# Kernel optimization log

Measured on AMD Instinct MI355X. Metric: run time of the kernel, lower is better.

## Reference

```python
import jax, jax.numpy as jnp
import numpy as np

B, S, H, V, T, NS, NB, NSW = 16, 200, 400, 25000, 8, 30, 3, 36


def setup_inputs() -> dict:
    key = jax.random.key(0)
    ks = jax.random.split(key, 12)
    return {
        "encoded_hidden": jax.random.normal(ks[0], (1, B, H), jnp.float32),
        "encoded_outputs": jax.random.normal(ks[1], (B, S, H), jnp.float32),
        "story": jax.random.randint(ks[2], (B, S), 0, V),
        "target_batches": jax.random.randint(ks[3], (B, NS, T), 0, V),
        "slot_dom_idx": jax.random.randint(ks[4], (NS,), 0, NSW),
        "slot_slot_idx": jax.random.randint(ks[5], (NS,), 0, NSW),
        "emb_W": jax.random.normal(ks[6], (V, H), jnp.float32) * 0.05,
        "slot_emb_W": jax.random.normal(ks[7], (NSW, H), jnp.float32) * 0.1,
        "gru_W_ih": jax.random.normal(ks[8], (3 * H, H), jnp.float32) * 0.05,
        "gru_W_hh": jax.random.normal(ks[9], (3 * H, H), jnp.float32) * 0.05,
        "gru_b_ih": jnp.zeros((3 * H,), jnp.float32),
        "gru_b_hh": jnp.zeros((3 * H,), jnp.float32),
        "W_ratio_w": jax.random.normal(ks[10], (1, 3 * H), jnp.float32) * 0.05,
        "W_ratio_b": jnp.zeros((1,), jnp.float32),
        "W_gate_w": jax.random.normal(ks[11], (NB, H), jnp.float32) * 0.05,
        "W_gate_b": jnp.zeros((NB,), jnp.float32),
    }


def reference(encoded_hidden, encoded_outputs, story, target_batches,
              slot_dom_idx, slot_slot_idx, emb_W, slot_emb_W,
              gru_W_ih, gru_W_hh, gru_b_ih, gru_b_hh,
              W_ratio_w, W_ratio_b, W_gate_w, W_gate_b):
    b, s, h = encoded_outputs.shape
    ns = slot_dom_idx.shape[0]
    v = emb_W.shape[0]
    t = target_batches.shape[2]
    bs = ns * b  # flattened slot*batch dim (parallel decode over slots)

    # slot embedding = domain_emb + slot_emb, broadcast over batch
    slot_emb = slot_emb_W[slot_dom_idx] + slot_emb_W[slot_slot_idx]        # [ns,h]
    dec_in0 = jnp.broadcast_to(slot_emb[:, None, :], (ns, b, h)).reshape(bs, h)
    h0 = jnp.tile(encoded_hidden[0], (ns, 1))                              # [bs,h]
    enc = jnp.tile(encoded_outputs, (ns, 1, 1))                            # [bs,s,h]
    pad_mask = jnp.tile(story == 0, (ns, 1))                               # [bs,s]
    story_rep = jnp.tile(story, (ns, 1))                                   # [bs,s]
    # teacher forcing targets, slot-major flatten: [bs, t]
    tf = jnp.transpose(target_batches, (1, 0, 2)).reshape(bs, t)
    rows = jnp.arange(bs)

    def gru_cell(x, hid):
        gx = x @ gru_W_ih.T + gru_b_ih
        gh = hid @ gru_W_hh.T + gru_b_hh
        r = jax.nn.sigmoid(gx[:, :h] + gh[:, :h])
        z = jax.nn.sigmoid(gx[:, h:2 * h] + gh[:, h:2 * h])
        n = jnp.tanh(gx[:, 2 * h:] + r * gh[:, 2 * h:])
        return (1.0 - z) * n + z * hid

    def step(carry, tgt_t):
        hid, x = carry
        hid = gru_cell(x, hid)                                             # [bs,h]
        scores = jnp.einsum('bh,bsh->bs', hid, enc)
        scores = jnp.where(pad_mask, -jnp.inf, scores)
        prob = jax.nn.softmax(scores, axis=1)                              # [bs,s]
        ctx = jnp.einsum('bs,bsh->bh', prob, enc)                          # [bs,h]
        p_vocab = jax.nn.softmax(hid @ emb_W.T, axis=1)                    # [bs,v]
        switch = jax.nn.sigmoid(
            jnp.concatenate([hid, ctx, x], axis=-1) @ W_ratio_w.T + W_ratio_b)  # [bs,1]
        p_ctx = jnp.zeros((bs, v), p_vocab.dtype).at[rows[:, None], story_rep].add(prob)
        final = (1.0 - switch) * p_ctx + switch * p_vocab                  # [bs,v]
        x_next = emb_W[tgt_t]                                              # teacher forcing
        return (hid, x_next), (final, ctx)

    (_, _), (finals, ctxs) = jax.lax.scan(step, (h0, dec_in0), tf.T)
    all_point = jnp.transpose(finals.reshape(t, ns, b, v), (1, 2, 0, 3))   # [ns,b,t,v]
    all_gate = (ctxs[0] @ W_gate_w.T + W_gate_b).reshape(ns, b, -1)        # [ns,b,nb_gate]
    return all_point, all_gate
```

## Files before the change

kernel.cpp:

```cpp
#include <hip/hip_runtime.h>
#include <math.h>

#define B_   16
#define S_   200
#define H_   400
#define V_   25000
#define T_   8
#define NS_  30
#define NB_  3
#define BS_  480

#define KP_  448
#define MP_  512
#define NP_  25088
#define NG_  1280
#define MA_  3840
#define NVT_ (NP_/128)
#define PSL_ 200

typedef unsigned short u16;
typedef __attribute__((ext_vector_type(4))) float f32x4;
typedef __attribute__((ext_vector_type(8))) short short8;

__device__ __forceinline__ u16 f2bf(float f) {
    unsigned u = __float_as_uint(f);
    u += 0x7FFFu + ((u >> 16) & 1u);
    return (u16)(u >> 16);
}
__device__ __forceinline__ float bf2f(u16 v) {
    return __uint_as_float(((unsigned)v) << 16);
}
__device__ __forceinline__ float sigm(float x) {
    return 1.f / (1.f + __expf(-x));
}
__device__ __forceinline__ float ftanh(float x) {
    float e2 = __expf(2.f * x);
    return 1.f - 2.f / (e2 + 1.f);
}
__device__ __forceinline__ float wred_sum(float v) {
    v += __shfl_xor(v, 32); v += __shfl_xor(v, 16); v += __shfl_xor(v, 8);
    v += __shfl_xor(v, 4);  v += __shfl_xor(v, 2);  v += __shfl_xor(v, 1);
    return v;
}
__device__ __forceinline__ float wred_max(float v) {
    v = fmaxf(v, __shfl_xor(v, 32)); v = fmaxf(v, __shfl_xor(v, 16));
    v = fmaxf(v, __shfl_xor(v, 8));  v = fmaxf(v, __shfl_xor(v, 4));
    v = fmaxf(v, __shfl_xor(v, 2));  v = fmaxf(v, __shfl_xor(v, 1));
    return v;
}
__device__ __forceinline__ void gload_lds16(const void* g, void* l) {
    __builtin_amdgcn_global_load_lds(
        (const __attribute__((address_space(1))) void*)g,
        (__attribute__((address_space(3))) void*)l, 16, 0, 0);
}

__device__ __forceinline__ void tile128(const u16* __restrict__ A, const u16* __restrict__ Bw,
                                        float* __restrict__ C, int m0, int n0, int Mlim, int Nlim,
                                        u16* As, u16* Bs, int tid) {
    const int wid = tid >> 6, lane = tid & 63;
    const int wr = wid >> 1, wc = wid & 1;
    f32x4 acc[4][4] = {};
    const int lcol = ((lane & 7) ^ ((lane >> 3) & 7)) * 8;
    const int lr = lane & 15, lg = lane >> 4, lx = lane & 7;
    const int sA0 = (lg ^ lx) * 8, sA1 = ((4 + lg) ^ lx) * 8;
    const u16* Ag = A + (size_t)(m0 + wid * 32 + (lane >> 3)) * KP_ + lcol;
    const u16* Bg = Bw + (size_t)(n0 + wid * 32 + (lane >> 3)) * KP_ + lcol;

    for (int kt = 0; kt < 7; ++kt) {
        const int k0 = kt * 64;
        #pragma unroll
        for (int is = 0; is < 4; ++is) {
            gload_lds16(Ag + (size_t)is * 8 * KP_ + k0, &As[(wid * 32 + is * 8) * 64]);
            gload_lds16(Bg + (size_t)is * 8 * KP_ + k0, &Bs[(wid * 32 + is * 8) * 64]);
        }
        __syncthreads();
        short8 af[4][2], bfr[4][2];
        #pragma unroll
        for (int i = 0; i < 4; ++i) {
            int ra = (wr * 64 + i * 16 + lr) * 64;
            af[i][0] = *reinterpret_cast<const short8*>(&As[ra + sA0]);
            af[i][1] = *reinterpret_cast<const short8*>(&As[ra + sA1]);
            int rb = (wc * 64 + i * 16 + lr) * 64;
            bfr[i][0] = *reinterpret_cast<const short8*>(&Bs[rb + sA0]);
            bfr[i][1] = *reinterpret_cast<const short8*>(&Bs[rb + sA1]);
        }
        #pragma unroll
        for (int h = 0; h < 2; ++h)
            #pragma unroll
            for (int i = 0; i < 4; ++i)
                #pragma unroll
                for (int j = 0; j < 4; ++j)
                    acc[i][j] = __builtin_amdgcn_mfma_f32_16x16x32_bf16(
                        af[i][h], bfr[j][h], acc[i][j], 0, 0, 0);
        __syncthreads();
    }
    const int m_base = m0 + wr * 64 + lg * 4;
    const int n_base = n0 + wc * 64 + lr;
    #pragma unroll
    for (int i = 0; i < 4; ++i)
        #pragma unroll
        for (int r = 0; r < 4; ++r) {
            int m = m_base + i * 16 + r;
            if (m >= Mlim) continue;
            #pragma unroll
            for (int j = 0; j < 4; ++j) {
                int n = n_base + j * 16;
                if (n < Nlim) C[(size_t)m * Nlim + n] = acc[i][j][r];
            }
        }
}

__global__ void prep_all(const float* __restrict__ eh, const float* __restrict__ embW,
                         const float* __restrict__ Wih, const float* __restrict__ Whh,
                         const float* __restrict__ sembW, const int* __restrict__ tb,
                         const int* __restrict__ dom, const int* __restrict__ sli,
                         float* __restrict__ hid, u16* __restrict__ Ab,
                         u16* __restrict__ Bb, u16* __restrict__ Wihb, u16* __restrict__ Whhb,
                         float* __restrict__ x_all, u16* __restrict__ Xb_all) {
    const int R0 = MP_ * KP_;
    const int CB = NP_ * (KP_ / 8), CG = NG_ * (KP_ / 8);
    const int R1 = R0 + CB + 2 * CG;
    const int R2 = R1 + MA_ * (KP_ / 8);
    int i = blockIdx.x * 256 + threadIdx.x;
    if (i < R0) {
        int row = i / KP_, d = i - row * KP_;
        u16 v = 0;
        if (row < BS_ && d < H_) {
            float h = eh[(row % B_) * H_ + d];
            hid[row * H_ + d] = h;
            v = f2bf(h);
        }
        Ab[i] = v;
    } else if (i < R1) {
        int j = i - R0;
        const float* src; u16* dst; int rows;
        if (j < CB) { src = embW; dst = Bb; rows = V_; }
        else if (j < CB + CG) { src = Wih; dst = Wihb; rows = 3 * H_; j -= CB; }
        else { src = Whh; dst = Whhb; rows = 3 * H_; j -= CB + CG; }
        int row = j / (KP_ / 8), c8 = (j - row * (KP_ / 8)) * 8;
        short8 o = {};
        if (row < rows && c8 < H_) {
            const float4* s = reinterpret_cast<const float4*>(src + (size_t)row * H_ + c8);
            float4 a = s[0], b = s[1];
            o[0] = (short)f2bf(a.x); o[1] = (short)f2bf(a.y);
            o[2] = (short)f2bf(a.z); o[3] = (short)f2bf(a.w);
            o[4] = (short)f2bf(b.x); o[5] = (short)f2bf(b.y);
            o[6] = (short)f2bf(b.z); o[7] = (short)f2bf(b.w);
        }
        *reinterpret_cast<short8*>(dst + (size_t)row * KP_ + c8) = o;
    } else if (i < R2) {
        int j = i - R1;
        int row = j / (KP_ / 8), c8 = (j - row * (KP_ / 8)) * 8;
        int t = row / BS_, r = row - t * BS_;
        int batch = r % B_, slot = r / B_;
        short8 o = {};
        if (c8 < H_) {
            float4 a, b;
            if (t == 0) {
                const float4* s0 = reinterpret_cast<const float4*>(sembW + dom[slot] * H_ + c8);
                const float4* s1 = reinterpret_cast<const float4*>(sembW + sli[slot] * H_ + c8);
                float4 x0 = s0[0], x1 = s0[1], y0 = s1[0], y1 = s1[1];
                a = make_float4(x0.x + y0.x, x0.y + y0.y, x0.z + y0.z, x0.w + y0.w);
                b = make_float4(x1.x + y1.x, x1.y + y1.y, x1.z + y1.z, x1.w + y1.w);
            } else {
                int tok = tb[(batch * NS_ + slot) * T_ + (t - 1)];
                const float4* s = reinterpret_cast<const float4*>(embW + (size_t)tok * H_ + c8);
                a = s[0]; b = s[1];
            }
            o[0] = (short)f2bf(a.x); o[1] = (short)f2bf(a.y);
            o[2] = (short)f2bf(a.z); o[3] = (short)f2bf(a.w);
            o[4] = (short)f2bf(b.x); o[5] = (short)f2bf(b.y);
            o[6] = (short)f2bf(b.z); o[7] = (short)f2bf(b.w);
            *reinterpret_cast<float4*>(x_all + (size_t)row * H_ + c8) = a;
            *reinterpret_cast<float4*>(x_all + (size_t)row * H_ + c8 + 4) = b;
        }
        *reinterpret_cast<short8*>(Xb_all + (size_t)row * KP_ + c8) = o;
    }
}

__global__ __launch_bounds__(256)
void gemm_setup(const u16* __restrict__ Xb_all, const u16* __restrict__ Abuf,
                const u16* __restrict__ Wihb, const u16* __restrict__ Whhb,
                float* __restrict__ gx_all, float* __restrict__ gh) {
    __shared__ u16 As[128 * 64];
    __shared__ u16 Bs[128 * 64];
    const int tid = threadIdx.x;
    const bool mainp = blockIdx.y < 4;
    const int m0 = (mainp ? blockIdx.y : blockIdx.y - 4) * 128;
    const int n0 = blockIdx.x * 128;
    if (mainp)
        tile128(Xb_all, Wihb, gx_all, m0, n0, MA_, 3 * H_, As, Bs, tid);
    else
        tile128(Abuf, Whhb, gh, m0, n0, BS_, 3 * H_, As, Bs, tid);
}

__global__ __launch_bounds__(256, 2)
void vocab_gh(const u16* __restrict__ A, const u16* __restrict__ Bb,
              const u16* __restrict__ Whhb, u16* __restrict__ pb,
              float* __restrict__ psum, float* __restrict__ gh,
              const u16* __restrict__ Xb_all, const u16* __restrict__ Wihb,
              float* __restrict__ gx_all) {
    __shared__ u16 As[256 * 64];
    __shared__ u16 Bs[2][128 * 64];
    __shared__ float sred[2][256];
    const int bid = blockIdx.x;
    const int tid = threadIdx.x;

    if (bid >= 412) {
        const int e = bid - 412;
        const int mt = 4 + e / 10, nt = e % 10;
        tile128(Xb_all, Wihb, gx_all, mt * 128, nt * 128, MA_, 3 * H_,
                As, (u16*)&Bs[0][0], tid);
        return;
    }

    const int xcd = bid & 7, idx = bid >> 3;
    const int lin = (xcd < 4) ? (xcd * 52 + idx) : (208 + (xcd - 4) * 51 + idx);
    const int ntall = lin >> 1, mt = lin & 1;
    const bool isv = (ntall < NVT_);
    const int n0 = (isv ? ntall : ntall - NVT_) * 128;
    const int m0 = mt * 256;
    const u16* Bsrc = isv ? Bb : Whhb;

    const int wid = tid >> 6, lane = tid & 63;
    const int wr = wid >> 1, wc = wid & 1;
    f32x4 acc[8][4] = {};
    const int lcol = ((lane & 7) ^ ((lane >> 3) & 7)) * 8;
    const int lr = lane & 15, lg = lane >> 4, lx = lane & 7;
    const int sA0 = (lg ^ lx) * 8, sA1 = ((4 + lg) ^ lx) * 8;
    const u16* Ag = A + (size_t)(m0 + wid * 64 + (lane >> 3)) * KP_ + lcol;
    const u16* Bg = Bsrc + (size_t)(n0 + wid * 32 + (lane >> 3)) * KP_ + lcol;

    #pragma unroll
    for (int is = 0; is < 4; ++is)
        gload_lds16(Bg + (size_t)is * 8 * KP_, &Bs[0][(wid * 32 + is * 8) * 64]);

    for (int kt = 0; kt < 7; ++kt) {
        const int k0 = kt * 64, cur = kt & 1;
        #pragma unroll
        for (int is = 0; is < 8; ++is)
            gload_lds16(Ag + (size_t)is * 8 * KP_ + k0, &As[(wid * 64 + is * 8) * 64]);
        if (kt < 6) {
            #pragma unroll
            for (int is = 0; is < 4; ++is)
                gload_lds16(Bg + (size_t)is * 8 * KP_ + k0 + 64,
                            &Bs[cur ^ 1][(wid * 32 + is * 8) * 64]);
            asm volatile("s_waitcnt vmcnt(4)" ::: "memory");
        } else {
            asm volatile("s_waitcnt vmcnt(0)" ::: "memory");
        }
        __builtin_amdgcn_sched_barrier(0);
        __builtin_amdgcn_s_barrier();
        const u16* Bsl = Bs[cur];
        #pragma unroll
        for (int h = 0; h < 2; ++h) {
            const int sA = h ? sA1 : sA0;
            short8 af[8], bf[4];
            #pragma unroll
            for (int i = 0; i < 8; ++i)
                af[i] = *reinterpret_cast<const short8*>(&As[(wr * 128 + i * 16 + lr) * 64 + sA]);
            #pragma unroll
            for (int j = 0; j < 4; ++j)
                bf[j] = *reinterpret_cast<const short8*>(&Bsl[(wc * 64 + j * 16 + lr) * 64 + sA]);
            #pragma unroll
            for (int i = 0; i < 8; ++i)
                #pragma unroll
                for (int j = 0; j < 4; ++j)
                    acc[i][j] = __builtin_amdgcn_mfma_f32_16x16x32_bf16(
                        af[i], bf[j], acc[i][j], 0, 0, 0);
        }
        __builtin_amdgcn_s_barrier();
    }

    const int m_base = m0 + wr * 128 + lg * 4;
    const int n_base = n0 + wc * 64 + lr;
    if (isv) {
        #pragma unroll
        for (int i = 0; i < 8; ++i) {
            #pragma unroll
            for (int r = 0; r < 4; ++r) {
                int m = m_base + i * 16 + r;
                float js = 0.f;
                #pragma unroll
                for (int j = 0; j < 4; ++j) {
                    int n = n_base + j * 16;
                    float e = __expf(acc[i][j][r]);
                    if (m < BS_ && n < V_) {
                        pb[(size_t)m * V_ + n] = f2bf(e);
                        js += e;
                    }
                }
                js += __shfl_xor(js, 1);
                js += __shfl_xor(js, 2);
                js += __shfl_xor(js, 4);
                js += __shfl_xor(js, 8);
                if ((lane & 15) == 0) sred[wc][m - m0] = js;
            }
        }
        __syncthreads();
        {
            int m = m0 + tid;
            psum[(size_t)m * PSL_ + ntall] = sred[0][tid] + sred[1][tid];
        }
    } else {
        #pragma unroll
        for (int i = 0; i < 8; ++i)
            #pragma unroll
            for (int r = 0; r < 4; ++r) {
                int m = m_base + i * 16 + r;
                if (m >= BS_) continue;
                #pragma unroll
                for (int j = 0; j < 4; ++j) {
                    int n = n_base + j * 16;
                    if (n < 3 * H_) gh[(size_t)m * 3 * H_ + n] = acc[i][j][r];
                }
            }
    }
}

__global__ __launch_bounds__(256)
void attn_fin(const float* __restrict__ gx_all, const float* __restrict__ gh,
              const float* __restrict__ bih, const float* __restrict__ bhh,
              float* __restrict__ hid, u16* __restrict__ Ab,
              const float* __restrict__ x_all,
              const float* __restrict__ enc, const int* __restrict__ story,
              const float* __restrict__ Wr, const float* __restrict__ Wrb,
              const float* __restrict__ Wg, const float* __restrict__ Wgb,
              float* __restrict__ prob_cur, float* __restrict__ sw_cur,
              float* __restrict__ gate_out,
              float* __restrict__ out, const u16* __restrict__ pb,
              const float* __restrict__ psum, const float* __restrict__ sw_prev,
              const float* __restrict__ prob_prev, int t) {
    const int bid = blockIdx.x;
    const int lin = (bid & 7) * 120 + (bid >> 3);
    const int work = lin >> 1, kind = lin & 1;
    const int tid = threadIdx.x, w = tid >> 6, l = tid & 63;
    __shared__ __align__(16) float hs[H_];
    __shared__ __align__(16) float xs[H_];
    __shared__ __align__(16) float cs[H_];
    __shared__ __align__(16) float cpart[4][H_];
    __shared__ float sc[S_];
    __shared__ float red[16];

    if (kind == 1) {
        if (t == 0) return;
        const int row = work, batch = row % B_;
        float rs = (tid < NVT_) ? psum[(size_t)row * PSL_ + tid] : 0.f;
        rs = wred_sum(rs);
        if (l == 0) red[w] = rs;
        __syncthreads();
        float denom = red[0] + red[1] + red[2] + red[3];
        float swv = sw_prev[row];
        float scl = swv / denom;
        const u16* ps = pb + (size_t)row * V_;
        float* p = out + ((size_t)row * T_ + (t - 1)) * V_;
        for (int v = tid * 8; v < V_; v += 256 * 8) {
            short8 in = *reinterpret_cast<const short8*>(ps + v);
            float4 o0, o1;
            o0.x = bf2f((u16)in[0]) * scl; o0.y = bf2f((u16)in[1]) * scl;
            o0.z = bf2f((u16)in[2]) * scl; o0.w = bf2f((u16)in[3]) * scl;
            o1.x = bf2f((u16)in[4]) * scl; o1.y = bf2f((u16)in[5]) * scl;
            o1.z = bf2f((u16)in[6]) * scl; o1.w = bf2f((u16)in[7]) * scl;
            *reinterpret_cast<float4*>(p + v) = o0;
            *reinterpret_cast<float4*>(p + v + 4) = o1;
        }
        __syncthreads();
        float om = 1.f - swv;
        for (int s = tid; s < S_; s += 256) {
            int tok = story[batch * S_ + s];
            atomicAdd(p + tok, om * prob_prev[(size_t)row * S_ + s]);
        }
        return;
    }

    const int batch = work / 30, slot = work - batch * 30;
    const int row = slot * B_ + batch;

    const float* gxr = gx_all + ((size_t)t * BS_ + row) * 3 * H_;
    const float* ghr = gh + (size_t)row * 3 * H_;
    const float* xr  = x_all + ((size_t)t * BS_ + row) * H_;
    for (int d = tid; d < H_; d += 256) {
        float r = sigm(gxr[d] + bih[d] + ghr[d] + bhh[d]);
        float z = sigm(gxr[H_ + d] + bih[H_ + d] + ghr[H_ + d] + bhh[H_ + d]);
        float n = ftanh(gxr[2 * H_ + d] + bih[2 * H_ + d] + r * (ghr[2 * H_ + d] + bhh[2 * H_ + d]));
        float h = (1.f - z) * n + z * hid[(size_t)row * H_ + d];
        hs[d] = h;
        hid[(size_t)row * H_ + d] = h;
        Ab[(size_t)row * KP_ + d] = f2bf(h);
        xs[d] = xr[d];
    }
    __syncthreads();

    const float* encb = enc + (size_t)batch * S_ * H_;
    {
        float4 hv1 = *reinterpret_cast<const float4*>(&hs[l * 4]);
        float4 hv2 = make_float4(0.f, 0.f, 0.f, 0.f);
        if (l < 36) hv2 = *reinterpret_cast<const float4*>(&hs[256 + l * 4]);
        for (int k = 0; k < 50; k += 2) {
            int s0 = w * 50 + k;
            const float4* e0 = reinterpret_cast<const float4*>(encb + (size_t)s0 * H_);
            const float4* e1 = reinterpret_cast<const float4*>(encb + (size_t)(s0 + 1) * H_);
            float4 ev0 = e0[l], ev1 = e1[l];
            float p0 = ev0.x * hv1.x + ev0.y * hv1.y + ev0.z * hv1.z + ev0.w * hv1.w;
            float p1 = ev1.x * hv1.x + ev1.y * hv1.y + ev1.z * hv1.z + ev1.w * hv1.w;
            if (l < 36) {
                float4 f0 = e0[64 + l], f1 = e1[64 + l];
                p0 += f0.x * hv2.x + f0.y * hv2.y + f0.z * hv2.z + f0.w * hv2.w;
                p1 += f1.x * hv2.x + f1.y * hv2.y + f1.z * hv2.z + f1.w * hv2.w;
            }
            p0 = wred_sum(p0);
            p1 = wred_sum(p1);
            if (l == 0) {
                sc[s0]     = (story[batch * S_ + s0] == 0)     ? -1e30f : p0;
                sc[s0 + 1] = (story[batch * S_ + s0 + 1] == 0) ? -1e30f : p1;
            }
        }
    }
    __syncthreads();

    float v = (tid < S_) ? sc[tid] : -1e30f;
    float wm = wred_max(v);
    if (l == 0) red[w] = wm;
    __syncthreads();
    float mx = fmaxf(fmaxf(red[0], red[1]), fmaxf(red[2], red[3]));
    float e = (tid < S_) ? __expf(v - mx) : 0.f;
    float wsum = wred_sum(e);
    if (l == 0) red[4 + w] = wsum;
    __syncthreads();
    float inv = 1.f / (red[4] + red[5] + red[6] + red[7]);
    if (tid < S_) {
        float pv = e * inv;
        sc[tid] = pv;
        prob_cur[(size_t)row * S_ + tid] = pv;
    }
    __syncthreads();

    {
        const int s0 = w * 50;
        for (int d = l; d < H_; d += 64) {
            float a0 = 0.f, a1 = 0.f;
            for (int k = 0; k < 50; k += 2) {
                a0 += sc[s0 + k]     * encb[(size_t)(s0 + k) * H_ + d];
                a1 += sc[s0 + k + 1] * encb[(size_t)(s0 + k + 1) * H_ + d];
            }
            cpart[w][d] = a0 + a1;
        }
    }
    __syncthreads();
    for (int d = tid; d < H_; d += 256)
        cs[d] = cpart[0][d] + cpart[1][d] + cpart[2][d] + cpart[3][d];
    __syncthreads();

    float part = 0.f;
    for (int i = tid; i < 3 * H_; i += 256) {
        float xv = (i < H_) ? hs[i] : (i < 2 * H_) ? cs[i - H_] : xs[i - 2 * H_];
        part += xv * Wr[i];
    }
    part = wred_sum(part);
    if (l == 0) red[8 + w] = part;
    __syncthreads();
    if (tid == 0)
        sw_cur[row] = sigm(red[8] + red[9] + red[10] + red[11] + Wrb[0]);

    if (t == 0 && tid < NB_) {
        float acc = 0.f;
        for (int d = 0; d < H_; ++d) acc += cs[d] * Wg[tid * H_ + d];
        gate_out[(size_t)row * NB_ + tid] = acc + Wgb[tid];
    }
}

__global__ __launch_bounds__(256)
void scale_scatter(float* __restrict__ out, const u16* __restrict__ pb,
                   const float* __restrict__ psum, const float* __restrict__ sw,
                   const float* __restrict__ prob, const int* __restrict__ story) {
    const int row = blockIdx.x;
    const int tid = threadIdx.x, w = tid >> 6, l = tid & 63;
    __shared__ float red[4];
    float rs = (tid < NVT_) ? psum[(size_t)row * PSL_ + tid] : 0.f;
    rs = wred_sum(rs);
    if (l == 0) red[w] = rs;
    __syncthreads();
    float denom = red[0] + red[1] + red[2] + red[3];
    float swv = sw[row];
    float scl = swv / denom;
    const u16* ps = pb + (size_t)row * V_;
    float* p = out + ((size_t)row * T_ + (T_ - 1)) * V_;
    for (int v = tid * 8; v < V_; v += 256 * 8) {
        short8 in = *reinterpret_cast<const short8*>(ps + v);
        float4 o0, o1;
        o0.x = bf2f((u16)in[0]) * scl; o0.y = bf2f((u16)in[1]) * scl;
        o0.z = bf2f((u16)in[2]) * scl; o0.w = bf2f((u16)in[3]) * scl;
        o1.x = bf2f((u16)in[4]) * scl; o1.y = bf2f((u16)in[5]) * scl;
        o1.z = bf2f((u16)in[6]) * scl; o1.w = bf2f((u16)in[7]) * scl;
        *reinterpret_cast<float4*>(p + v) = o0;
        *reinterpret_cast<float4*>(p + v + 4) = o1;
    }
    __syncthreads();
    const int batch = row % B_;
    float om = 1.f - swv;
    for (int s = tid; s < S_; s += 256) {
        int tok = story[batch * S_ + s];
        atomicAdd(p + tok, om * prob[(size_t)row * S_ + s]);
    }
}

extern "C" void kernel_launch(void* const* d_in, const int* in_sizes, int n_in,
                              void* d_out, int out_size, void* d_ws, size_t ws_size,
                              hipStream_t stream) {
    const float* eh    = (const float*)d_in[0];
    const float* enc   = (const float*)d_in[1];
    const int*   story = (const int*)d_in[2];
    const int*   tb    = (const int*)d_in[3];
    const int*   dom   = (const int*)d_in[4];
    const int*   sli   = (const int*)d_in[5];
    const float* embW  = (const float*)d_in[6];
    const float* sembW = (const float*)d_in[7];
    const float* Wih   = (const float*)d_in[8];
    const float* Whh   = (const float*)d_in[9];
    const float* bih   = (const float*)d_in[10];
    const float* bhh   = (const float*)d_in[11];
    const float* Wr    = (const float*)d_in[12];
    const float* Wrb   = (const float*)d_in[13];
    const float* Wg    = (const float*)d_in[14];
    const float* Wgb   = (const float*)d_in[15];

    float* out = (float*)d_out;
    float* ws  = (float*)d_ws;

    float* gx_all = ws;
    float* gh     = gx_all + (size_t)MA_ * 3 * H_;
    float* hid    = gh + (size_t)BS_ * 3 * H_;
    float* x_all  = hid + (size_t)BS_ * H_;
    float* prob2  = x_all + (size_t)MA_ * H_;
    float* sw2    = prob2 + 2 * BS_ * S_;
    float* psum   = sw2 + 2 * BS_;
    u16* Ab     = (u16*)(psum + (size_t)MP_ * PSL_);
    u16* Xb_all = Ab + (size_t)MP_ * KP_;
    u16* Wihb   = Xb_all + (size_t)MA_ * KP_;
    u16* Whhb   = Wihb + (size_t)NG_ * KP_;
    u16* Bb     = Whhb + (size_t)NG_ * KP_;
    u16* pb     = Bb + (size_t)NP_ * KP_;
    size_t need = (size_t)((char*)(pb + (size_t)BS_ * V_) - (char*)ws);
    if (ws_size < need) return;

    float* gate_out = out + (size_t)NS_ * B_ * T_ * V_;

    {
        const int R2 = MP_ * KP_ + (NP_ + 2 * NG_) * (KP_ / 8) + MA_ * (KP_ / 8);
        prep_all<<<(R2 + 255) / 256, 256, 0, stream>>>(eh, embW, Wih, Whh, sembW, tb, dom, sli,
                                                       hid, Ab, Bb, Wihb, Whhb, x_all, Xb_all);
    }
    gemm_setup<<<dim3(NG_ / 128, 8), 256, 0, stream>>>(Xb_all, Ab, Wihb, Whhb, gx_all, gh);

    for (int t = 0; t < T_; ++t) {
        const int cur = t & 1, prev = cur ^ 1;
        attn_fin<<<960, 256, 0, stream>>>(gx_all, gh, bih, bhh, hid, Ab, x_all,
                                          enc, story, Wr, Wrb, Wg, Wgb,
                                          prob2 + cur * BS_ * S_, sw2 + cur * BS_,
                                          gate_out, out, pb, psum,
                                          sw2 + prev * BS_, prob2 + prev * BS_ * S_, t);
        vocab_gh<<<(t == 0 ? 672 : 412), 256, 0, stream>>>(Ab, Bb, Whhb, pb, psum, gh,
                                                           Xb_all, Wihb, gx_all);
    }
    {
        const int last = (T_ - 1) & 1;
        scale_scatter<<<BS_, 256, 0, stream>>>(out, pb, psum, sw2 + last * BS_,
                                               prob2 + last * BS_ * S_, story);
    }
}
```

Before: 776.7 us.

## Stage vocab exp tile in LDS for coalesced stores; move gx GEMM to setup

Result: faster. 758.5 us (-2.3%).

```diff
diff --git a/kernel.cpp b/kernel.cpp
--- a/kernel.cpp
+++ b/kernel.cpp
@@ -21,6 +21,7 @@
 typedef unsigned short u16;
 typedef __attribute__((ext_vector_type(4))) float f32x4;
 typedef __attribute__((ext_vector_type(8))) short short8;
+typedef __attribute__((ext_vector_type(4))) short short4v;
 
 __device__ __forceinline__ u16 f2bf(float f) {
     unsigned u = __float_as_uint(f);
@@ -185,8 +186,8 @@
     __shared__ u16 As[128 * 64];
     __shared__ u16 Bs[128 * 64];
     const int tid = threadIdx.x;
-    const bool mainp = blockIdx.y < 4;
-    const int m0 = (mainp ? blockIdx.y : blockIdx.y - 4) * 128;
+    const bool mainp = blockIdx.y < (MA_ / 128);
+    const int m0 = (mainp ? blockIdx.y : blockIdx.y - MA_ / 128) * 128;
     const int n0 = blockIdx.x * 128;
     if (mainp)
         tile128(Xb_all, Wihb, gx_all, m0, n0, MA_, 3 * H_, As, Bs, tid);
@@ -197,23 +198,14 @@
 __global__ __launch_bounds__(256, 2)
 void vocab_gh(const u16* __restrict__ A, const u16* __restrict__ Bb,
               const u16* __restrict__ Whhb, u16* __restrict__ pb,
-              float* __restrict__ psum, float* __restrict__ gh,
-              const u16* __restrict__ Xb_all, const u16* __restrict__ Wihb,
-              float* __restrict__ gx_all) {
-    __shared__ u16 As[256 * 64];
-    __shared__ u16 Bs[2][128 * 64];
+              float* __restrict__ psum, float* __restrict__ gh) {
+    __shared__ u16 SM[256 * 64 + 2 * 128 * 64];
     __shared__ float sred[2][256];
+    u16* As  = SM;
+    u16* Bs0 = SM + 256 * 64;
+    u16* Bs1 = SM + 256 * 64 + 128 * 64;
     const int bid = blockIdx.x;
     const int tid = threadIdx.x;
-
-    if (bid >= 412) {
-        const int e = bid - 412;
-        const int mt = 4 + e / 10, nt = e % 10;
-        tile128(Xb_all, Wihb, gx_all, mt * 128, nt * 128, MA_, 3 * H_,
-                As, (u16*)&Bs[0][0], tid);
-        return;
-    }
-
     const int xcd = bid & 7, idx = bid >> 3;
     const int lin = (xcd < 4) ? (xcd * 52 + idx) : (208 + (xcd - 4) * 51 + idx);
     const int ntall = lin >> 1, mt = lin & 1;
@@ -233,7 +225,7 @@
 
     #pragma unroll
     for (int is = 0; is < 4; ++is)
-        gload_lds16(Bg + (size_t)is * 8 * KP_, &Bs[0][(wid * 32 + is * 8) * 64]);
+        gload_lds16(Bg + (size_t)is * 8 * KP_, &Bs0[(wid * 32 + is * 8) * 64]);
 
     for (int kt = 0; kt < 7; ++kt) {
         const int k0 = kt * 64, cur = kt & 1;
@@ -241,17 +233,18 @@
         for (int is = 0; is < 8; ++is)
             gload_lds16(Ag + (size_t)is * 8 * KP_ + k0, &As[(wid * 64 + is * 8) * 64]);
         if (kt < 6) {
+            u16* Bnxt = cur ? Bs0 : Bs1;
             #pragma unroll
             for (int is = 0; is < 4; ++is)
                 gload_lds16(Bg + (size_t)is * 8 * KP_ + k0 + 64,
-                            &Bs[cur ^ 1][(wid * 32 + is * 8) * 64]);
+                            &Bnxt[(wid * 32 + is * 8) * 64]);
             asm volatile("s_waitcnt vmcnt(4)" ::: "memory");
         } else {
             asm volatile("s_waitcnt vmcnt(0)" ::: "memory");
         }
         __builtin_amdgcn_sched_barrier(0);
         __builtin_amdgcn_s_barrier();
-        const u16* Bsl = Bs[cur];
+        const u16* Bsl = cur ? Bs1 : Bs0;
         #pragma unroll
         for (int h = 0; h < 2; ++h) {
             const int sA = h ? sA1 : sA0;
@@ -272,29 +265,26 @@
         __builtin_amdgcn_s_barrier();
     }
 
-    const int m_base = m0 + wr * 128 + lg * 4;
-    const int n_base = n0 + wc * 64 + lr;
     if (isv) {
+        u16* pbs = SM;
         #pragma unroll
         for (int i = 0; i < 8; ++i) {
             #pragma unroll
             for (int r = 0; r < 4; ++r) {
-                int m = m_base + i * 16 + r;
+                const int mloc = wr * 128 + i * 16 + lg * 4 + r;
                 float js = 0.f;
                 #pragma unroll
                 for (int j = 0; j < 4; ++j) {
-                    int n = n_base + j * 16;
+                    const int nloc = wc * 64 + j * 16 + lr;
                     float e = __expf(acc[i][j][r]);
-                    if (m < BS_ && n < V_) {
-                        pb[(size_t)m * V_ + n] = f2bf(e);
-                        js += e;
-                    }
+                    pbs[mloc * 128 + nloc] = f2bf(e);
+                    if (m0 + mloc < BS_ && n0 + nloc < V_) js += e;
                 }
                 js += __shfl_xor(js, 1);
                 js += __shfl_xor(js, 2);
                 js += __shfl_xor(js, 4);
                 js += __shfl_xor(js, 8);
-                if ((lane & 15) == 0) sred[wc][m - m0] = js;
+                if ((lane & 15) == 0) sred[wc][mloc] = js;
             }
         }
         __syncthreads();
@@ -302,7 +292,16 @@
             int m = m0 + tid;
             psum[(size_t)m * PSL_ + ntall] = sred[0][tid] + sred[1][tid];
         }
+        const int mmax = BS_ - m0;
+        for (int c = tid; c < 256 * 16; c += 256) {
+            const int mloc = c >> 4, c8 = (c & 15) * 8;
+            if (mloc < mmax && n0 + c8 + 8 <= V_)
+                *reinterpret_cast<short8*>(pb + (size_t)(m0 + mloc) * V_ + n0 + c8) =
+                    *reinterpret_cast<const short8*>(pbs + mloc * 128 + c8);
+        }
     } else {
+        const int m_base = m0 + wr * 128 + lg * 4;
+        const int n_base = n0 + wc * 64 + lr;
         #pragma unroll
         for (int i = 0; i < 8; ++i)
             #pragma unroll
@@ -354,15 +353,12 @@
         float scl = swv / denom;
         const u16* ps = pb + (size_t)row * V_;
         float* p = out + ((size_t)row * T_ + (t - 1)) * V_;
-        for (int v = tid * 8; v < V_; v += 256 * 8) {
-            short8 in = *reinterpret_cast<const short8*>(ps + v);
-            float4 o0, o1;
-            o0.x = bf2f((u16)in[0]) * scl; o0.y = bf2f((u16)in[1]) * scl;
-            o0.z = bf2f((u16)in[2]) * scl; o0.w = bf2f((u16)in[3]) * scl;
-            o1.x = bf2f((u16)in[4]) * scl; o1.y = bf2f((u16)in[5]) * scl;
-            o1.z = bf2f((u16)in[6]) * scl; o1.w = bf2f((u16)in[7]) * scl;
-            *reinterpret_cast<float4*>(p + v) = o0;
-            *reinterpret_cast<float4*>(p + v + 4) = o1;
+        for (int v = tid * 4; v < V_; v += 1024) {
+            short4v in = *reinterpret_cast<const short4v*>(ps + v);
+            float4 o;
+            o.x = bf2f((u16)in[0]) * scl; o.y = bf2f((u16)in[1]) * scl;
+            o.z = bf2f((u16)in[2]) * scl; o.w = bf2f((u16)in[3]) * scl;
+            *reinterpret_cast<float4*>(p + v) = o;
         }
         __syncthreads();
         float om = 1.f - swv;
@@ -485,15 +481,12 @@
     float scl = swv / denom;
     const u16* ps = pb + (size_t)row * V_;
     float* p = out + ((size_t)row * T_ + (T_ - 1)) * V_;
-    for (int v = tid * 8; v < V_; v += 256 * 8) {
-        short8 in = *reinterpret_cast<const short8*>(ps + v);
-        float4 o0, o1;
-        o0.x = bf2f((u16)in[0]) * scl; o0.y = bf2f((u16)in[1]) * scl;
-        o0.z = bf2f((u16)in[2]) * scl; o0.w = bf2f((u16)in[3]) * scl;
-        o1.x = bf2f((u16)in[4]) * scl; o1.y = bf2f((u16)in[5]) * scl;
-        o1.z = bf2f((u16)in[6]) * scl; o1.w = bf2f((u16)in[7]) * scl;
-        *reinterpret_cast<float4*>(p + v) = o0;
-        *reinterpret_cast<float4*>(p + v + 4) = o1;
+    for (int v = tid * 4; v < V_; v += 1024) {
+        short4v in = *reinterpret_cast<const short4v*>(ps + v);
+        float4 o;
+        o.x = bf2f((u16)in[0]) * scl; o.y = bf2f((u16)in[1]) * scl;
+        o.z = bf2f((u16)in[2]) * scl; o.w = bf2f((u16)in[3]) * scl;
+        *reinterpret_cast<float4*>(p + v) = o;
     }
     __syncthreads();
     const int batch = row % B_;
@@ -550,7 +543,8 @@
         prep_all<<<(R2 + 255) / 256, 256, 0, stream>>>(eh, embW, Wih, Whh, sembW, tb, dom, sli,
                                                        hid, Ab, Bb, Wihb, Whhb, x_all, Xb_all);
     }
-    gemm_setup<<<dim3(NG_ / 128, 8), 256, 0, stream>>>(Xb_all, Ab, Wihb, Whhb, gx_all, gh);
+    gemm_setup<<<dim3(NG_ / 128, MA_ / 128 + MP_ / 128), 256, 0, stream>>>(
+        Xb_all, Ab, Wihb, Whhb, gx_all, gh);
 
     for (int t = 0; t < T_; ++t) {
         const int cur = t & 1, prev = cur ^ 1;
@@ -559,8 +553,7 @@
                                           prob2 + cur * BS_ * S_, sw2 + cur * BS_,
                                           gate_out, out, pb, psum,
                                           sw2 + prev * BS_, prob2 + prev * BS_ * S_, t);
-        vocab_gh<<<(t == 0 ? 672 : 412), 256, 0, stream>>>(Ab, Bb, Whhb, pb, psum, gh,
-                                                           Xb_all, Wihb, gx_all);
+        vocab_gh<<<412, 256, 0, stream>>>(Ab, Bb, Whhb, pb, psum, gh);
     }
     {
         const int last = (T_ - 1) & 1;
```
